# Kernel tuning notes

Hardware: AMD Instinct MI355X
Metric: run time of the kernel (lower is better)

Reference implementation:

```python
import jax, jax.numpy as jnp
import numpy as np
from jax import lax

# norse LIFParameters defaults: dt=1e-3, tau_mem_inv=100, tau_syn_inv=200, v_leak=0, v_reset=0
ALPHA = 100.0
DT_TM = 0.1   # dt * tau_mem_inv
DT_TS = 0.2   # dt * tau_syn_inv

@jax.custom_vjp
def superspike(x):
    # Heaviside forward, SuperSpike surrogate gradient backward
    return (x > 0).astype(x.dtype)

def _ss_fwd(x):
    return superspike(x), x

def _ss_bwd(x, g):
    return (g / (ALPHA * jnp.abs(x) + 1.0) ** 2,)

superspike.defvjp(_ss_fwd, _ss_bwd)

def lif_step(inp, v, i, v_th):
    # norse lif_feed_forward_step (feedforward LIF cell)
    v_dec = v + DT_TM * (i - v)           # v_leak = 0
    i_dec = i * (1.0 - DT_TS)
    z = superspike(v_dec - v_th)
    v_new = (1.0 - z) * v_dec             # reset to v_reset = 0 on spike
    return z, v_new, i_dec + inp

def conv2d(x, w):
    return lax.conv_general_dilated(x, w, (1, 1), 'VALID',
                                    dimension_numbers=('NCHW', 'OIHW', 'NCHW'))

def avg_pool2(x):
    s = lax.reduce_window(x, jnp.zeros((), x.dtype), lax.add,
                          (1, 1, 2, 2), (1, 1, 2, 2), 'VALID')
    return s * jnp.asarray(0.25, x.dtype)

def setup_inputs() -> dict:
    key = jax.random.key(0)
    ks = jax.random.split(key, 6)
    x = jax.random.uniform(ks[0], (40, 256, 1, 28, 28), dtype=jnp.float32)
    # kaiming-ish scales (1/sqrt(fan_in))
    w_conv1 = jax.random.normal(ks[1], (20, 1, 3, 3), jnp.float32) * (1.0 / np.sqrt(9))
    w_conv2 = jax.random.normal(ks[2], (50, 20, 3, 3), jnp.float32) * (1.0 / np.sqrt(180))
    w_fc1 = jax.random.normal(ks[3], (500, 6050), jnp.float32) * (1.0 / np.sqrt(6050))
    w_fc2 = jax.random.normal(ks[4], (200, 500), jnp.float32) * (1.0 / np.sqrt(500))
    w_fc_out = jax.random.normal(ks[5], (10, 200), jnp.float32) * (1.0 / np.sqrt(200))
    return {"x": x, "w_conv1": w_conv1, "w_conv2": w_conv2,
            "w_fc1": w_fc1, "w_fc2": w_fc2, "w_fc_out": w_fc_out}

def reference(x, w_conv1, w_conv2, w_fc1, w_fc2, w_fc_out):
    T, B = x.shape[0], x.shape[1]
    dt = x.dtype
    z0 = jnp.zeros((B, 20, 26, 26), dt)
    z1 = jnp.zeros((B, 50, 11, 11), dt)
    z2 = jnp.zeros((B, 500), dt)
    z3 = jnp.zeros((B, 200), dt)
    zo = jnp.zeros((B, 10), dt)
    carry0 = (z0, z0, z1, z1, z2, z2, z3, z3, zo, zo)

    def step(carry, xt):
        v0, i0, v1, i1, v2, i2, v3, i3, vo, io = carry
        z = conv2d(xt, w_conv1)
        z, v0, i0 = lif_step(z, v0, i0, 0.2)
        z = avg_pool2(z)
        z = conv2d(z, w_conv2)
        z, v1, i1 = lif_step(z, v1, i1, 0.2)
        z = z.reshape(B, -1)                      # [B, 50*11*11]
        z = z @ w_fc1.T
        z, v2, i2 = lif_step(z, v2, i2, 0.1)
        z = z @ w_fc2.T
        z, v3, i3 = lif_step(z, v3, i3, 0.05)
        z = z @ w_fc_out.T
        # LICell (norse li_feed_forward_step): output is decayed membrane voltage
        v_dec = vo + DT_TM * (io - vo)
        i_new = io * (1.0 - DT_TS) + z
        return (v0, i0, v1, i1, v2, i2, v3, i3, v_dec, i_new), v_dec

    _, voltages = lax.scan(step, carry0, x)
    return voltages  # [T, B, output_neurons]
```

## Files before the change

### kernel.cpp

```cpp
#include <hip/hip_runtime.h>
#include <hip/hip_bf16.h>

typedef _Float16 f16x8 __attribute__((ext_vector_type(8)));
typedef float f32x4  __attribute__((ext_vector_type(4)));
typedef unsigned short u16x4 __attribute__((ext_vector_type(4)));

#define T_STEPS 40
#define BATCH   256
#define S2LO    0.000244140625f

__device__ __forceinline__ unsigned short f2h_bits(float f) {
    union { _Float16 h; unsigned short u; } c; c.h = (_Float16)f; return c.u;
}

__device__ __forceinline__ float lif_update(float inp, float& v, float& i, float vth) {
    float vd = __fadd_rn(v, __fmul_rn(0.1f, __fsub_rn(i, v)));
    float id = __fmul_rn(0.8f, i);
    float z  = (vd > vth) ? 1.0f : 0.0f;
    v = (vd > vth) ? 0.0f : vd;
    i = __fadd_rn(id, inp);
    return z;
}

__device__ __forceinline__ void llds16(const unsigned short* g, void* l) {
    __builtin_amdgcn_global_load_lds(
        (const __attribute__((address_space(1))) unsigned int*)g,
        (__attribute__((address_space(3))) unsigned int*)l, 16, 0, 0);
}

__global__ __launch_bounds__(512) void k_conv1(
    const float* __restrict__ x,
    const float* __restrict__ w1,
    unsigned char* __restrict__ s0)
{
    const int b    = blockIdx.y;
    const int tid  = threadIdx.x;
    const int cell = blockIdx.x*512 + tid;
    const bool active = cell < 3380;
    const int pos  = cell / 20;
    const int oc   = cell % 20;
    const int pr   = pos / 13, q = pos % 13;
    const int r0   = 2*pr, c0 = 2*q;

    __shared__ __align__(16) float xl[2][784];

    float wr[9];
    if (active) {
        #pragma unroll
        for (int j = 0; j < 9; ++j) wr[j] = w1[oc*9 + j];
    }
    float vs[2][2], is[2][2];
    #pragma unroll
    for (int dr = 0; dr < 2; ++dr)
        #pragma unroll
        for (int dc = 0; dc < 2; ++dc) { vs[dr][dc] = 0.f; is[dr][dc] = 0.f; }

    if (tid < 196) {
        const float4* xs4 = (const float4*)(x + (size_t)b*784);
        *(float4*)&xl[0][tid*4] = xs4[tid];
    }

    for (int t = 0; t < T_STEPS; ++t) {
        __syncthreads();
        if (t + 1 < T_STEPS && tid < 196) {
            const float4* xs4 = (const float4*)(x + (size_t)((t+1)*BATCH + b)*784);
            *(float4*)&xl[(t+1)&1][tid*4] = xs4[tid];
        }
        const float* xc = xl[t&1];
        size_t base = (size_t)(t*BATCH + b) * 4096;

        if (active) {
            float tle[4][4];
            #pragma unroll
            for (int r = 0; r < 4; ++r)
                #pragma unroll
                for (int c = 0; c < 4; ++c)
                    tle[r][c] = xc[(r0 + r)*28 + c0 + c];
            int zsum = 0;
            #pragma unroll
            for (int dr = 0; dr < 2; ++dr)
                #pragma unroll
                for (int dc = 0; dc < 2; ++dc) {
                    float acc = 0.f;
                    #pragma unroll
                    for (int kr = 0; kr < 3; ++kr)
                        #pragma unroll
                        for (int kc = 0; kc < 3; ++kc)
                            acc += tle[dr+kr][dc+kc] * wr[kr*3+kc];
                    float z = lif_update(acc, vs[dr][dc], is[dr][dc], 0.2f);
                    zsum += (z > 0.5f) ? 1 : 0;
                }
            s0[base + (size_t)pos*24 + oc] = (unsigned char)zsum;
        } else {
            int p2 = cell - 3380;
            for (int idx = p2; idx < 716; idx += 204) {
                if (idx < 676) s0[base + (size_t)(idx >> 2)*24 + 20 + (idx & 3)] = 0;
                else           s0[base + 4056 + (idx - 676)] = 0;
            }
        }
    }
}

__global__ __launch_bounds__(256, 2) void k_conv2(
    const unsigned char* __restrict__ s0,
    const float* __restrict__ w2,
    unsigned short* __restrict__ z1)
{
    const int b    = blockIdx.x >> 1;
    const int half = blockIdx.x & 1;
    const int tid  = threadIdx.x;
    const int wv   = tid >> 6;
    const int lane = tid & 63;
    const int l15  = lane & 15;
    const int kg   = lane >> 4;
    const int wm   = wv;

    __shared__ __align__(16) unsigned short w2h[32*232];
    __shared__ __align__(16) unsigned short w2m[32*232];
    __shared__ __align__(16) unsigned short sIn[2*4096];

    for (int s = tid; s < 32*232; s += 256) {
        int ocw = s / 232, kk = s % 232;
        int g = kk / 24, ic = kk % 24;
        int oc = half*32 + ocw;
        float val = 0.f;
        if (oc < 50 && g < 9 && ic < 20) val = w2[(oc*20 + ic)*9 + g];
        _Float16 h = (_Float16)val;
        float r1 = (val - (float)h) * 4096.0f;
        union { _Float16 h; unsigned short u; } ch, cm;
        ch.h = h; cm.h = (_Float16)r1;
        w2h[s] = ch.u;
        w2m[s] = cm.u;
    }

    f16x8 bfrH[2][7];
    int addrA[2][7];
    #pragma unroll
    for (int mt = 0; mt < 2; ++mt) {
        int pos = wm*32 + mt*16 + l15;
        #pragma unroll
        for (int kt = 0; kt < 7; ++kt) {
            int k = kt*32 + kg*8;
            int g = k / 24, o = k - g*24;
            if (pos <= 120 && g <= 8) {
                int in_idx = pos + 2*(pos/11) + 13*(g/3) + (g % 3);
                addrA[mt][kt] = in_idx*48 + o*2;
            } else addrA[mt][kt] = 8128;
        }
    }

    {
        const unsigned char* srow = s0 + (size_t)(0*BATCH + b)*4096;
        uint4 raw = *(const uint4*)(srow + tid*16);
        unsigned short hv[16];
        #pragma unroll
        for (int w = 0; w < 4; ++w) {
            unsigned int u = ((const unsigned int*)&raw)[w];
            #pragma unroll
            for (int j = 0; j < 4; ++j)
                hv[w*4+j] = f2h_bits(0.25f * (float)((u >> (8*j)) & 0xFFu));
        }
        unsigned short* dst = sIn + tid*16;
        *(f16x8*)dst       = *(const f16x8*)&hv[0];
        *(f16x8*)(dst + 8) = *(const f16x8*)&hv[8];
    }
    __syncthreads();

    #pragma unroll
    for (int nt = 0; nt < 2; ++nt) {
        int n = nt*16 + l15;
        #pragma unroll
        for (int kt = 0; kt < 7; ++kt)
            bfrH[nt][kt] = *(const f16x8*)&w2h[n*232 + kt*32 + kg*8];
    }

    float vst[2][2][4], ist[2][2][4];
    #pragma unroll
    for (int mt = 0; mt < 2; ++mt)
        #pragma unroll
        for (int nt = 0; nt < 2; ++nt)
            #pragma unroll
            for (int r = 0; r < 4; ++r) { vst[mt][nt][r] = 0.f; ist[mt][nt][r] = 0.f; }

    const f32x4 zero4 = {0.f, 0.f, 0.f, 0.f};

    for (int t = 0; t < T_STEPS; ++t) {
        if (t > 0) __syncthreads();

        uint4 raw;
        if (t + 1 < T_STEPS)
            raw = *(const uint4*)(s0 + (size_t)((t+1)*BATCH + b)*4096 + tid*16);

        const char* curB = (const char*)(sIn + (t&1)*4096);

        f32x4 acch[2][2], accl[2][2];
        #pragma unroll
        for (int mt = 0; mt < 2; ++mt)
            #pragma unroll
            for (int nt = 0; nt < 2; ++nt) { acch[mt][nt] = zero4; accl[mt][nt] = zero4; }

        #pragma unroll
        for (int kt = 0; kt < 7; ++kt) {
            f16x8 bm[2];
            #pragma unroll
            for (int nt = 0; nt < 2; ++nt) {
                int n = nt*16 + l15, k = kt*32 + kg*8;
                bm[nt] = *(const f16x8*)&w2m[n*232 + k];
            }
            #pragma unroll
            for (int mt = 0; mt < 2; ++mt) {
                f16x8 a = *(const f16x8*)(curB + addrA[mt][kt]);
                #pragma unroll
                for (int nt = 0; nt < 2; ++nt) {
                    acch[mt][nt] = __builtin_amdgcn_mfma_f32_16x16x32_f16(
                        a, bfrH[nt][kt], acch[mt][nt], 0, 0, 0);
                    accl[mt][nt] = __builtin_amdgcn_mfma_f32_16x16x32_f16(
                        a, bm[nt], accl[mt][nt], 0, 0, 0);
                }
            }
        }

        size_t rowoff = (size_t)(t*BATCH + b) * 6208;
        #pragma unroll
        for (int mt = 0; mt < 2; ++mt) {
            int posb = wm*32 + mt*16 + kg*4;
            #pragma unroll
            for (int nt = 0; nt < 2; ++nt) {
                int ocn = half*32 + nt*16 + l15;
                u16x4 pack;
                #pragma unroll
                for (int r = 0; r < 4; ++r) {
                    float inp = __fadd_rn(acch[mt][nt][r], __fmul_rn(S2LO, accl[mt][nt][r]));
                    float z = lif_update(inp, vst[mt][nt][r], ist[mt][nt][r], 0.2f);
                    int pos = posb + r;
                    pack[r] = (pos <= 120 && z > 0.5f) ? (unsigned short)0x3C00 : (unsigned short)0;
                }
                if (ocn < 50 && posb < 121)
                    *(u16x4*)(z1 + rowoff + ocn*124 + posb) = pack;
            }
        }
        if (half == 0 && tid < 8) z1[rowoff + 6200 + tid] = 0;

        if (t + 1 < T_STEPS) {
            unsigned short hv[16];
            #pragma unroll
            for (int w = 0; w < 4; ++w) {
                unsigned int u = ((const unsigned int*)&raw)[w];
                #pragma unroll
                for (int j = 0; j < 4; ++j)
                    hv[w*4+j] = f2h_bits(0.25f * (float)((u >> (8*j)) & 0xFFu));
            }
            unsigned short* dst = sIn + ((t+1)&1)*4096 + tid*16;
            *(f16x8*)dst       = *(const f16x8*)&hv[0];
            *(f16x8*)(dst + 8) = *(const f16x8*)&hv[8];
        }
    }
}

__global__ __launch_bounds__(256, 4) void k_gemm_fc1(
    const unsigned short* __restrict__ A,
    const unsigned short* __restrict__ Bhi,
    const unsigned short* __restrict__ Blo,
    float* __restrict__ P)
{
    __shared__ __align__(16) unsigned short As[128*64];
    __shared__ __align__(16) unsigned short Bh[64*64];
    __shared__ __align__(16) unsigned short Bl[64*64];

    const int tid  = threadIdx.x;
    const int lane = tid & 63;
    const int wv   = tid >> 6;
    const int wm   = wv & 1, wn = wv >> 1;
    const int l15  = lane & 15, kg = lane >> 4;
    const int mbase = blockIdx.x * 128;
    const int nbase = blockIdx.y * 64;
    const int kz    = blockIdx.z;
    const int kb0   = kz * 3136;
    const int kiters = 49 - kz;

    float* Pz = P + (size_t)kz * 5242880;

    const f32x4 zero4 = {0.f, 0.f, 0.f, 0.f};
    f32x4 acch[4][2], accl[4][2];
    #pragma unroll
    for (int mt = 0; mt < 4; ++mt)
        #pragma unroll
        for (int nt = 0; nt < 2; ++nt) { acch[mt][nt] = zero4; accl[mt][nt] = zero4; }

    const int rowA = tid >> 3;
    const int sw   = (((tid & 7) ^ (rowA & 7))) * 8;
    char* ldsA = (char*)As + (size_t)wv*1024;
    char* ldsH = (char*)Bh + (size_t)wv*1024;
    char* ldsL = (char*)Bl + (size_t)wv*1024;

    for (int ki = 0; ki < kiters; ++ki) {
        int kb = kb0 + ki * 64;
        #pragma unroll
        for (int c = 0; c < 4; ++c)
            llds16(A + (size_t)(mbase + c*32 + rowA)*6208 + kb + sw, ldsA + c*4096);
        #pragma unroll
        for (int c = 0; c < 2; ++c) {
            llds16(Bhi + (size_t)(nbase + c*32 + rowA)*6208 + kb + sw, ldsH + c*4096);
            llds16(Blo + (size_t)(nbase + c*32 + rowA)*6208 + kb + sw, ldsL + c*4096);
        }
        __syncthreads();
        #pragma unroll
        for (int kt = 0; kt < 2; ++kt) {
            f16x8 bh[2], bl[2], afv[4];
            #pragma unroll
            for (int nt = 0; nt < 2; ++nt) {
                int rb = wn*32 + nt*16 + l15;
                int ch = ((kt*4 + kg) ^ (rb & 7)) * 8;
                bh[nt] = *(const f16x8*)&Bh[rb*64 + ch];
                bl[nt] = *(const f16x8*)&Bl[rb*64 + ch];
            }
            #pragma unroll
            for (int mt = 0; mt < 4; ++mt) {
                int ra = wm*64 + mt*16 + l15;
                int ch = ((kt*4 + kg) ^ (ra & 7)) * 8;
                afv[mt] = *(const f16x8*)&As[ra*64 + ch];
            }
            #pragma unroll
            for (int mt = 0; mt < 4; ++mt)
                #pragma unroll
                for (int nt = 0; nt < 2; ++nt) {
                    acch[mt][nt] = __builtin_amdgcn_mfma_f32_16x16x32_f16(
                        afv[mt], bh[nt], acch[mt][nt], 0, 0, 0);
                    accl[mt][nt] = __builtin_amdgcn_mfma_f32_16x16x32_f16(
                        afv[mt], bl[nt], accl[mt][nt], 0, 0, 0);
                }
        }
        __syncthreads();
    }

    #pragma unroll
    for (int mt = 0; mt < 4; ++mt) {
        int m0 = mbase + wm*64 + mt*16 + kg*4;
        #pragma unroll
        for (int nt = 0; nt < 2; ++nt) {
            int n = nbase + wn*32 + nt*16 + l15;
            #pragma unroll
            for (int r = 0; r < 4; ++r) {
                float s = __fadd_rn(acch[mt][nt][r], __fmul_rn(S2LO, accl[mt][nt][r]));
                Pz[(size_t)(m0 + r)*512 + n] = s;
            }
        }
    }
}

__global__ __launch_bounds__(256, 3) void k_gemm(
    const unsigned short* __restrict__ A,
    const unsigned short* __restrict__ B0,
    float* __restrict__ C0,
    int Kp, int kiters, int ldc, int nstore,
    size_t strideB, size_t strideC)
{
    __shared__ __align__(16) unsigned short As[128*64];
    __shared__ __align__(16) unsigned short Bs[128*64];
    const unsigned short* B = B0 + (size_t)blockIdx.z * strideB;
    float* C = C0 + (size_t)blockIdx.z * strideC;

    const int tid  = threadIdx.x;
    const int lane = tid & 63;
    const int wv   = tid >> 6;
    const int wm   = wv & 1, wn = wv >> 1;
    const int l15  = lane & 15, kg = lane >> 4;
    const int mbase = blockIdx.x * 128;
    const int nbase = blockIdx.y * 128;

    const f32x4 zero4 = {0.f, 0.f, 0.f, 0.f};
    f32x4 acc[4][4];
    #pragma unroll
    for (int mt = 0; mt < 4; ++mt)
        #pragma unroll
        for (int nt = 0; nt < 4; ++nt) acc[mt][nt] = zero4;

    const int rowA = tid >> 3;
    const int sw   = (((tid & 7) ^ (rowA & 7))) * 8;
    char* ldsA = (char*)As + (size_t)wv*1024;
    char* ldsB = (char*)Bs + (size_t)wv*1024;

    for (int ki = 0; ki < kiters; ++ki) {
        int kb = ki * 64;
        #pragma unroll
        for (int c = 0; c < 4; ++c) {
            int row = c*32 + rowA;
            llds16(A + (size_t)(mbase + row)*Kp + kb + sw, ldsA + c*4096);
            llds16(B + (size_t)(nbase + row)*Kp + kb + sw, ldsB + c*4096);
        }
        __syncthreads();
        #pragma unroll
        for (int kt = 0; kt < 2; ++kt) {
            f16x8 bfv[4], afv[4];
            #pragma unroll
            for (int nt = 0; nt < 4; ++nt) {
                int rb = wn*64 + nt*16 + l15;
                int ch = ((kt*4 + kg) ^ (rb & 7)) * 8;
                bfv[nt] = *(const f16x8*)&Bs[rb*64 + ch];
            }
            #pragma unroll
            for (int mt = 0; mt < 4; ++mt) {
                int ra = wm*64 + mt*16 + l15;
                int ch = ((kt*4 + kg) ^ (ra & 7)) * 8;
                afv[mt] = *(const f16x8*)&As[ra*64 + ch];
            }
            #pragma unroll
            for (int mt = 0; mt < 4; ++mt)
                #pragma unroll
                for (int nt = 0; nt < 4; ++nt)
                    acc[mt][nt] = __builtin_amdgcn_mfma_f32_16x16x32_f16(
                        afv[mt], bfv[nt], acc[mt][nt], 0, 0, 0);
        }
        __syncthreads();
    }

    #pragma unroll
    for (int mt = 0; mt < 4; ++mt) {
        int m0 = mbase + wm*64 + mt*16 + kg*4;
        #pragma unroll
        for (int nt = 0; nt < 4; ++nt) {
            int n = nbase + wn*64 + nt*16 + l15;
            if (n < nstore) {
                #pragma unroll
                for (int r = 0; r < 4; ++r)
                    C[(size_t)(m0 + r)*ldc + n] = acc[mt][nt][r];
            }
        }
    }
}

__global__ void k_pack(const float* __restrict__ src,
                       unsigned short* __restrict__ hi, unsigned short* __restrict__ lo,
                       int N, int K, int Kp, int total) {
    int idx = blockIdx.x*256 + threadIdx.x;
    if (idx >= total) return;
    int n = idx / Kp, k = idx - n*Kp;
    float v = (n < N && k < K) ? src[n*K + k] : 0.f;
    _Float16 h = (_Float16)v;
    float r1 = (v - (float)h) * 4096.0f;
    union { _Float16 h; unsigned short u; } ch, cl;
    ch.h = h; cl.h = (_Float16)r1;
    hi[idx] = ch.u;
    lo[idx] = cl.u;
}

__global__ void k_pack_fc1(const float* __restrict__ src,
                           unsigned short* __restrict__ hi, unsigned short* __restrict__ lo,
                           int total) {
    int idx = blockIdx.x*256 + threadIdx.x;
    if (idx >= total) return;
    int n = idx / 6208, k = idx - n*6208;
    int oc = k / 124, pos = k - oc*124;
    float v = (n < 500 && oc < 50 && pos < 121) ? src[n*6050 + oc*121 + pos] : 0.f;
    _Float16 h = (_Float16)v;
    float r1 = (v - (float)h) * 4096.0f;
    union { _Float16 h; unsigned short u; } ch, cl;
    ch.h = h; cl.h = (_Float16)r1;
    hi[idx] = ch.u;
    lo[idx] = cl.u;
}

__global__ __launch_bounds__(512) void k_lif_scan(
    const float* __restrict__ c0, size_t pstride,
    unsigned short* __restrict__ zout,
    int ld, int nvalid, float vth, float pscale)
{
    int b = blockIdx.x;
    int n = threadIdx.x;
    float v = 0.f, cur = 0.f;
    for (int t = 0; t < T_STEPS; ++t) {
        size_t idx = (size_t)(t*BATCH + b)*ld + n;
        float s = __fadd_rn(c0[idx], __fmul_rn(pscale, c0[idx + pstride]));
        float z = lif_update(s, v, cur, vth);
        zout[idx] = (n < nvalid && z > 0.5f) ? (unsigned short)0x3C00 : (unsigned short)0;
    }
}

__global__ void k_li(const float* __restrict__ c0, size_t pstride, float* __restrict__ out) {
    int g = blockIdx.x*64 + threadIdx.x;
    if (g >= 2560) return;
    int b = g / 10, n = g - b*10;
    float vo = 0.f, io = 0.f;
    for (int t = 0; t < T_STEPS; ++t) {
        size_t idx = (size_t)(t*BATCH + b)*16 + n;
        float s = __fadd_rn(c0[idx], __fmul_rn(S2LO, c0[idx + pstride]));
        float vd = __fadd_rn(vo, __fmul_rn(0.1f, __fsub_rn(io, vo)));
        out[(size_t)(t*BATCH + b)*10 + n] = vd;
        io = __fadd_rn(__fmul_rn(0.8f, io), s);
        vo = vd;
    }
}

extern "C" void kernel_launch(void* const* d_in, const int* in_sizes, int n_in,
                              void* d_out, int out_size, void* d_ws, size_t ws_size,
                              hipStream_t stream) {
    (void)in_sizes; (void)n_in; (void)out_size; (void)ws_size;
    const float* x   = (const float*)d_in[0];
    const float* w1  = (const float*)d_in[1];
    const float* w2  = (const float*)d_in[2];
    const float* wf1 = (const float*)d_in[3];
    const float* wf2 = (const float*)d_in[4];
    const float* wfo = (const float*)d_in[5];
    char* ws = (char*)d_ws;

    unsigned short* z1    = (unsigned short*)(ws);
    unsigned char*  s0    = (unsigned char*)(ws + 127139840);
    unsigned short* W1hi  = (unsigned short*)(ws + 127139840);
    unsigned short* W2hi  = (unsigned short*)(ws + 139853824);
    unsigned short* Wohi  = (unsigned short*)(ws + 140378112);
    float*          c2p   = (float*)(ws + 140509184);
    unsigned short* z2    = (unsigned short*)(ws);
    float*          c3p   = (float*)(ws + 10485760);
    unsigned short* z3    = (unsigned short*)(ws + 31457280);
    float*          c4p   = (float*)(ws + 36700160);

    k_conv1<<<dim3(7, 256), 512, 0, stream>>>(x, w1, s0);
    k_conv2<<<512, 256, 0, stream>>>(s0, w2, z1);

    k_pack_fc1<<<(3178496+255)/256, 256, 0, stream>>>(wf1, W1hi, W1hi+3178496, 3178496);
    k_pack<<<(131072+255)/256, 256, 0, stream>>>(wf2, W2hi, W2hi+131072, 200, 500, 512, 131072);
    k_pack<<<(32768+255)/256,  256, 0, stream>>>(wfo, Wohi, Wohi+32768,  10,  200, 256, 32768);

    k_gemm_fc1<<<dim3(80, 8, 2), 256, 0, stream>>>(z1, W1hi, W1hi+3178496, c2p);
    k_lif_scan<<<256, 512, 0, stream>>>(c2p, (size_t)5242880, z2, 512, 500, 0.1f, 1.0f);
    k_gemm<<<dim3(80,2,2), 256, 0, stream>>>(z2, W2hi, c3p, 512, 8, 256, 256,
                                             (size_t)131072, (size_t)2621440);
    k_lif_scan<<<256, 256, 0, stream>>>(c3p, (size_t)2621440, z3, 256, 200, 0.05f, S2LO);
    k_gemm<<<dim3(80,1,2), 256, 0, stream>>>(z3, Wohi, c4p, 256, 4, 16, 16,
                                             (size_t)32768, (size_t)163840);
    k_li<<<40, 64, 0, stream>>>(c4p, (size_t)163840, (float*)d_out);
}
```

Baseline: 408.4 us.

## Interleave split-K partials, remap fc1 grid for XCD locality, prefetch scan loads

GEMM partial results from the two K-splits (or hi/lo halves) are now stored interleaved as float2 pairs instead of in separate planes, so the LIF and LI scan kernels load both with one 8-byte access. The fc1 GEMM moves to a 1D grid whose block index is remapped so that consecutive blocks sent to the same XCD share A/B tiles and L2 reuse improves. The scan kernels are unrolled by four with loads issued four timesteps ahead to hide global-memory latency in the serial time recurrence. The tradeoff is strided GEMM epilogue stores, each of which fills only half of every 8-byte pair.

```diff
diff --git a/kernel.cpp b/kernel.cpp
--- a/kernel.cpp
+++ b/kernel.cpp
@@ -272,13 +272,16 @@
     const int wv   = tid >> 6;
     const int wm   = wv & 1, wn = wv >> 1;
     const int l15  = lane & 15, kg = lane >> 4;
-    const int mbase = blockIdx.x * 128;
-    const int nbase = blockIdx.y * 64;
-    const int kz    = blockIdx.z;
+
+    const int bid   = blockIdx.x;
+    const int chunk = (bid & 7) * 160 + (bid >> 3);
+    const int mb    = chunk >> 4;
+    const int nn    = chunk & 15;
+    const int mbase = mb * 128;
+    const int nbase = (nn >> 1) * 64;
+    const int kz    = nn & 1;
     const int kb0   = kz * 3136;
     const int kiters = 49 - kz;
-
-    float* Pz = P + (size_t)kz * 5242880;
 
     const f32x4 zero4 = {0.f, 0.f, 0.f, 0.f};
     f32x4 acch[4][2], accl[4][2];
@@ -342,7 +345,7 @@
             #pragma unroll
             for (int r = 0; r < 4; ++r) {
                 float s = __fadd_rn(acch[mt][nt][r], __fmul_rn(S2LO, accl[mt][nt][r]));
-                Pz[(size_t)(m0 + r)*512 + n] = s;
+                P[((size_t)(m0 + r)*512 + n)*2 + kz] = s;
             }
         }
     }
@@ -353,12 +356,12 @@
     const unsigned short* __restrict__ B0,
     float* __restrict__ C0,
     int Kp, int kiters, int ldc, int nstore,
-    size_t strideB, size_t strideC)
+    size_t strideB)
 {
     __shared__ __align__(16) unsigned short As[128*64];
     __shared__ __align__(16) unsigned short Bs[128*64];
-    const unsigned short* B = B0 + (size_t)blockIdx.z * strideB;
-    float* C = C0 + (size_t)blockIdx.z * strideC;
+    const int z = blockIdx.z;
+    const unsigned short* B = B0 + (size_t)z * strideB;
 
     const int tid  = threadIdx.x;
     const int lane = tid & 63;
@@ -423,7 +426,7 @@
             if (n < nstore) {
                 #pragma unroll
                 for (int r = 0; r < 4; ++r)
-                    C[(size_t)(m0 + r)*ldc + n] = acc[mt][nt][r];
+                    C0[((size_t)(m0 + r)*ldc + n)*2 + z] = acc[mt][nt][r];
             }
         }
     }
@@ -461,34 +464,63 @@
 }
 
 __global__ __launch_bounds__(512) void k_lif_scan(
-    const float* __restrict__ c0, size_t pstride,
+    const float* __restrict__ c0,
     unsigned short* __restrict__ zout,
     int ld, int nvalid, float vth, float pscale)
 {
     int b = blockIdx.x;
     int n = threadIdx.x;
     float v = 0.f, cur = 0.f;
-    for (int t = 0; t < T_STEPS; ++t) {
-        size_t idx = (size_t)(t*BATCH + b)*ld + n;
-        float s = __fadd_rn(c0[idx], __fmul_rn(pscale, c0[idx + pstride]));
-        float z = lif_update(s, v, cur, vth);
-        zout[idx] = (n < nvalid && z > 0.5f) ? (unsigned short)0x3C00 : (unsigned short)0;
-    }
-}
-
-__global__ void k_li(const float* __restrict__ c0, size_t pstride, float* __restrict__ out) {
+    const float2* src = (const float2*)c0 + (size_t)b*ld + n;
+    const size_t step = (size_t)BATCH*ld;
+    float2 p0 = src[0], p1 = src[step], p2 = src[2*step], p3 = src[3*step];
+
+    #define LIF_SUB(J, PV, NEXTLOAD)                                          \
+        {                                                                     \
+            float s = __fadd_rn(PV.x, __fmul_rn(pscale, PV.y));               \
+            float z = lif_update(s, v, cur, vth);                             \
+            zout[(size_t)((t+J)*BATCH + b)*ld + n] =                          \
+                (n < nvalid && z > 0.5f) ? (unsigned short)0x3C00             \
+                                         : (unsigned short)0;                 \
+            if (t + J + 4 < T_STEPS) PV = src[(size_t)(t + J + 4)*step];      \
+            (void)0; NEXTLOAD;                                                \
+        }
+
+    for (int t = 0; t < T_STEPS; t += 4) {
+        LIF_SUB(0, p0, );
+        LIF_SUB(1, p1, );
+        LIF_SUB(2, p2, );
+        LIF_SUB(3, p3, );
+    }
+    #undef LIF_SUB
+}
+
+__global__ void k_li(const float* __restrict__ c0, float* __restrict__ out) {
     int g = blockIdx.x*64 + threadIdx.x;
     if (g >= 2560) return;
     int b = g / 10, n = g - b*10;
+    const float2* src = (const float2*)c0 + (size_t)b*16 + n;
+    const size_t step = (size_t)BATCH*16;
     float vo = 0.f, io = 0.f;
-    for (int t = 0; t < T_STEPS; ++t) {
-        size_t idx = (size_t)(t*BATCH + b)*16 + n;
-        float s = __fadd_rn(c0[idx], __fmul_rn(S2LO, c0[idx + pstride]));
-        float vd = __fadd_rn(vo, __fmul_rn(0.1f, __fsub_rn(io, vo)));
-        out[(size_t)(t*BATCH + b)*10 + n] = vd;
-        io = __fadd_rn(__fmul_rn(0.8f, io), s);
-        vo = vd;
-    }
+    float2 p0 = src[0], p1 = src[step], p2 = src[2*step], p3 = src[3*step];
+
+    #define LI_SUB(J, PV)                                                     \
+        {                                                                     \
+            float s = __fadd_rn(PV.x, __fmul_rn(S2LO, PV.y));                 \
+            float vd = __fadd_rn(vo, __fmul_rn(0.1f, __fsub_rn(io, vo)));     \
+            out[(size_t)((t+J)*BATCH + b)*10 + n] = vd;                       \
+            io = __fadd_rn(__fmul_rn(0.8f, io), s);                           \
+            vo = vd;                                                          \
+            if (t + J + 4 < T_STEPS) PV = src[(size_t)(t + J + 4)*step];      \
+        }
+
+    for (int t = 0; t < T_STEPS; t += 4) {
+        LI_SUB(0, p0);
+        LI_SUB(1, p1);
+        LI_SUB(2, p2);
+        LI_SUB(3, p3);
+    }
+    #undef LI_SUB
 }
 
 extern "C" void kernel_launch(void* const* d_in, const int* in_sizes, int n_in,
@@ -521,12 +553,12 @@
     k_pack<<<(131072+255)/256, 256, 0, stream>>>(wf2, W2hi, W2hi+131072, 200, 500, 512, 131072);
     k_pack<<<(32768+255)/256,  256, 0, stream>>>(wfo, Wohi, Wohi+32768,  10,  200, 256, 32768);
 
-    k_gemm_fc1<<<dim3(80, 8, 2), 256, 0, stream>>>(z1, W1hi, W1hi+3178496, c2p);
-    k_lif_scan<<<256, 512, 0, stream>>>(c2p, (size_t)5242880, z2, 512, 500, 0.1f, 1.0f);
+    k_gemm_fc1<<<1280, 256, 0, stream>>>(z1, W1hi, W1hi+3178496, c2p);
+    k_lif_scan<<<256, 512, 0, stream>>>(c2p, z2, 512, 500, 0.1f, 1.0f);
     k_gemm<<<dim3(80,2,2), 256, 0, stream>>>(z2, W2hi, c3p, 512, 8, 256, 256,
-                                             (size_t)131072, (size_t)2621440);
-    k_lif_scan<<<256, 256, 0, stream>>>(c3p, (size_t)2621440, z3, 256, 200, 0.05f, S2LO);
+                                             (size_t)131072);
+    k_lif_scan<<<256, 256, 0, stream>>>(c3p, z3, 256, 200, 0.05f, S2LO);
     k_gemm<<<dim3(80,1,2), 256, 0, stream>>>(z3, Wohi, c4p, 256, 4, 16, 16,
-                                             (size_t)32768, (size_t)163840);
-    k_li<<<40, 64, 0, stream>>>(c4p, (size_t)163840, (float*)d_out);
-}
+                                             (size_t)32768);
+    k_li<<<40, 64, 0, stream>>>(c4p, (float*)d_out);
+}
```

Result: slower. 421.0 us (+3.1%).
